# Kernel optimization log

Hardware: AMD Instinct MI355X
Metric: run time of the kernel (lower is better)

Reference implementation:

```python
import jax, jax.numpy as jnp
import numpy as np

# NTM hyperparams (must match init_kwargs)
U = 256        # controller units
N = 128        # memory locations
M = 64         # memory vector size
R = 1          # read heads
WH = 1         # write heads
SHIFT = 1      # conv shift range
S = 2 * SHIFT + 1
OUT = 8        # num_bits_per_vector
CLIP = 20.0
IN_DIM = OUT + 1  # copy task input channels
H = R + WH
PER = M + 1 + 1 + S + 1           # k, beta, g, s, gamma per head
P = H * PER + WH * 2 * M          # + erase/add per write head


def setup_inputs() -> dict:
    key = jax.random.key(0)
    ks = jax.random.split(key, 10)
    B, T = 128, 130
    ctrl_in = IN_DIM + R * M
    def gn(k, shape, fan_in):
        return jax.random.normal(k, shape, jnp.float32) / jnp.sqrt(jnp.float32(fan_in))
    return {
        "inputs": (jax.random.uniform(ks[0], (B, T, IN_DIM)) > 0.5).astype(jnp.float32),
        "W_x": gn(ks[1], (ctrl_in, 4 * U), ctrl_in),
        "W_h": gn(ks[2], (U, 4 * U), U),
        "b_lstm": jnp.zeros((4 * U,), jnp.float32),
        "W_p": gn(ks[3], (U, P), U),
        "b_p": jnp.zeros((P,), jnp.float32),
        "W_o": gn(ks[4], (U + R * M, OUT), U + R * M),
        "b_o": jnp.zeros((OUT,), jnp.float32),
        "r0": jax.random.normal(ks[5], (R, M), jnp.float32) * 0.1,
        "w0": jax.random.normal(ks[6], (H, N), jnp.float32) * 0.1,
        "max_seq_len": 64,
    }


def _ntm_forward(inputs, W_x, W_h, b_lstm, W_p, b_p, W_o, b_o, r0, w0):
    B, T, _ = inputs.shape
    # constant-init memory, learned init read vectors / weightings
    Mem0 = jnp.full((B, N, M), 1e-6, jnp.float32)
    r_prev0 = jnp.broadcast_to(jnp.tanh(r0)[None], (B, R, M))
    w_prev0 = jnp.broadcast_to(jax.nn.softmax(w0, axis=-1)[None], (B, H, N))
    h0 = jnp.zeros((B, U), jnp.float32)
    c0 = jnp.zeros((B, U), jnp.float32)

    def step(carry, x_t):
        h, c, r_prev, w_prev, Mem = carry
        # controller LSTM (input = x_t ++ prev read vectors)
        ctrl_in = jnp.concatenate([x_t, r_prev.reshape(B, R * M)], axis=-1)
        gates = ctrl_in @ W_x + h @ W_h + b_lstm
        i, f, g_, o = jnp.split(gates, 4, axis=-1)
        c = jax.nn.sigmoid(f) * c + jax.nn.sigmoid(i) * jnp.tanh(g_)
        h = jax.nn.sigmoid(o) * jnp.tanh(c)
        # head parameters
        params = jnp.clip(h @ W_p + b_p, -CLIP, CLIP)
        hp = params[:, : H * PER].reshape(B, H, PER)
        k = jnp.tanh(hp[..., :M])                              # [B,H,M]
        beta = jax.nn.softplus(hp[..., M])[..., None]          # [B,H,1]
        g = jax.nn.sigmoid(hp[..., M + 1])[..., None]          # [B,H,1]
        s = jax.nn.softmax(hp[..., M + 2 : M + 2 + S], axis=-1)  # [B,H,S]
        gamma = (1.0 + jax.nn.softplus(hp[..., M + 2 + S]))[..., None]  # [B,H,1]
        ea = params[:, H * PER :].reshape(B, WH, 2, M)
        erase = jax.nn.sigmoid(ea[:, :, 0])                    # [B,WH,M]
        add = jnp.tanh(ea[:, :, 1])                            # [B,WH,M]
        # content addressing: cosine similarity
        inner = jnp.einsum("bhm,bnm->bhn", k, Mem)
        kn = jnp.linalg.norm(k, axis=-1, keepdims=True)        # [B,H,1]
        Mn = jnp.linalg.norm(Mem, axis=-1)[:, None, :]         # [B,1,N]
        K = inner / (kn * Mn + 1e-8)
        w_c = jax.nn.softmax(beta * K, axis=-1)                # [B,H,N]
        # interpolation
        w_g = g * w_c + (1.0 - g) * w_prev
        # circular convolutional shift
        w_tilde = jnp.zeros_like(w_g)
        for d in range(-SHIFT, SHIFT + 1):
            w_tilde = w_tilde + s[..., d + SHIFT : d + SHIFT + 1] * jnp.roll(w_g, d, axis=-1)
        # sharpening
        w_pow = w_tilde ** gamma
        w = w_pow / (jnp.sum(w_pow, axis=-1, keepdims=True) + 1e-8)
        w_r, w_w = w[:, :R], w[:, R:]
        # write (sequential over write heads)
        for j in range(WH):
            ww = w_w[:, j, :, None]                            # [B,N,1]
            Mem = Mem * (1.0 - ww * erase[:, j, None, :]) + ww * add[:, j, None, :]
        # read
        r = jnp.einsum("brn,bnm->brm", w_r, Mem)
        out = jnp.clip(jnp.concatenate([h, r.reshape(B, R * M)], axis=-1) @ W_o + b_o, -CLIP, CLIP)
        return (h, c, r, w, Mem), out

    xs = jnp.swapaxes(inputs, 0, 1)  # [T,B,IN]
    _, outs = jax.lax.scan(step, (h0, c0, r_prev0, w_prev0, Mem0), xs)
    return jnp.swapaxes(outs, 0, 1)  # [B,T,OUT]


def reference(inputs, W_x, W_h, b_lstm, W_p, b_p, W_o, b_o, r0, w0, max_seq_len):
    seq = _ntm_forward(inputs, W_x, W_h, b_lstm, W_p, b_p, W_o, b_o, r0, w0)
    logits = seq[:, max_seq_len + 1 :, :]  # copy task slice
    return jax.nn.sigmoid(logits)
```

## Files before the change

kernel.cpp:

```cpp
#include <hip/hip_runtime.h>
#include <math.h>

typedef _Float16 h2_t __attribute__((ext_vector_type(2)));

#define U_ 256
#define NN 128
#define MM 64
#define OUT_ 8
#define CLIPV 20.0f
#define IN_DIM_ 9
#define PP 268
#define B_ 128
#define T_ 130
#define TSTART 65

#define NWX2 10240
#define NWH8 16384
#define NWP8 4352
#define WX2_OFF 0
#define WH8_OFF 163840
#define WP8_OFF 425984
#define BLH_OFF 495616
#define BPP_OFF 499712
#define COMM_OFF 500800
#define COMM_STRIDE 2176
#define COMM_SZ (B_*COMM_STRIDE)
#define PREP_N (NWX2 + NWH8 + NWP8 + 256 + 272)

#define WSCALE 256.f
#define HSCALE 127.f
#define OSCALE (1.f/(256.f*127.f))

__device__ __forceinline__ float sigf(float x){ return 1.0f/(1.0f+__expf(-x)); }
__device__ __forceinline__ float splus(float x){ return log1pf(__expf(x)); }
__device__ __forceinline__ float clipf(float x){ return fminf(fmaxf(x,-CLIPV),CLIPV); }

#if defined(__has_builtin)
#if __has_builtin(__builtin_amdgcn_fdot2)
#define DOT2(a,b,c) __builtin_amdgcn_fdot2((a),(b),(c),false)
#endif
#endif
#ifndef DOT2
#define DOT2(a,b,c) fmaf((float)(a).x,(float)(b).x, fmaf((float)(a).y,(float)(b).y,(c)))
#endif

#if defined(__has_builtin)
#if __has_builtin(__builtin_amdgcn_sdot4)
#define SDOT4(a,b,c) __builtin_amdgcn_sdot4((a),(b),(c),false)
#endif
#endif
#ifndef SDOT4
__device__ __forceinline__ int sdot4_sw(int a, int b, int c){
    c += (int)(signed char)(a      ) * (int)(signed char)(b      );
    c += (int)(signed char)(a >> 8 ) * (int)(signed char)(b >> 8 );
    c += (int)(signed char)(a >> 16) * (int)(signed char)(b >> 16);
    c += (a >> 24) * (b >> 24);
    return c;
}
#define SDOT4(a,b,c) sdot4_sw((a),(b),(c))
#endif

#define DOT2X4(uu, hv) { \
    a0 = DOT2(hv, __builtin_bit_cast(h2_t,(uu).x), a0); \
    a1 = DOT2(hv, __builtin_bit_cast(h2_t,(uu).y), a1); \
    a2 = DOT2(hv, __builtin_bit_cast(h2_t,(uu).z), a2); \
    a3 = DOT2(hv, __builtin_bit_cast(h2_t,(uu).w), a3); }
#define SD4(u, hw) { \
    a0 = SDOT4((int)(u).x, hw, a0); a1 = SDOT4((int)(u).y, hw, a1); \
    a2 = SDOT4((int)(u).z, hw, a2); a3 = SDOT4((int)(u).w, hw, a3); }
#define SD4P(u, hw) { \
    pa0 = SDOT4((int)(u).x, hw, pa0); pa1 = SDOT4((int)(u).y, hw, pa1); \
    pa2 = SDOT4((int)(u).z, hw, pa2); pa3 = SDOT4((int)(u).w, hw, pa3); }
#define H2C(hu) __builtin_bit_cast(h2_t,(hu))

__device__ __forceinline__ unsigned packh2(float a, float b){
    h2_t v; v.x = (_Float16)a; v.y = (_Float16)b;
    return __builtin_bit_cast(unsigned, v);
}

__device__ __forceinline__ unsigned ei8(float w){
    int v = (int)rintf(w * WSCALE);
    v = v < -127 ? -127 : (v > 127 ? 127 : v);
    return (unsigned)(v & 0xFF);
}

__device__ __forceinline__ unsigned packi8x4(float a, float b, float c, float d){
    int va = (int)rintf(a * HSCALE); va = va < -127 ? -127 : (va > 127 ? 127 : va);
    int vb = (int)rintf(b * HSCALE); vb = vb < -127 ? -127 : (vb > 127 ? 127 : vb);
    int vc = (int)rintf(c * HSCALE); vc = vc < -127 ? -127 : (vc > 127 ? 127 : vc);
    int vd = (int)rintf(d * HSCALE); vd = vd < -127 ? -127 : (vd > 127 ? 127 : vd);
    return (va & 0xFF) | ((vb & 0xFF) << 8) | ((vc & 0xFF) << 16) | ((vd & 0xFF) << 24);
}

__global__ void prep_kernel(const float* __restrict__ W_x, const float* __restrict__ W_h,
                            const float* __restrict__ W_p, const float* __restrict__ b_lstm,
                            const float* __restrict__ b_p,
                            uint4* __restrict__ wx2, uint4* __restrict__ whi8,
                            uint4* __restrict__ wpi8,
                            float4* __restrict__ blh, float* __restrict__ bpp)
{
    for (int idx = blockIdx.x*blockDim.x + threadIdx.x; idx < PREP_N; idx += gridDim.x*blockDim.x){
        if (idx < NWX2){
            int hf = idx/5120, rem = idx - hf*5120;
            int wv = rem/320, r2 = rem - wv*320, p = r2>>6, ln = r2&63;
            int g4 = wv*8 + (ln>>3), q = ln&7, kk = q*5+p;
            int k0 = 2*kk, k1 = k0+1;
            unsigned c[4];
            #pragma unroll
            for (int g=0; g<4; ++g){
                int col = g*256 + hf*128 + g4;
                float f0 = (k0<64) ? W_x[(9+k0)*1024+col] : (k0<73 ? W_x[(k0-64)*1024+col] : 0.f);
                float f1 = (k1<64) ? W_x[(9+k1)*1024+col] : (k1<73 ? W_x[(k1-64)*1024+col] : 0.f);
                c[g] = packh2(f0,f1);
            }
            wx2[idx] = make_uint4(c[0],c[1],c[2],c[3]);
        } else if (idx < NWX2 + NWH8){
            int e = idx - NWX2;
            int hf = e>>13, rem = e&8191, g4 = rem>>6, s = rem&63;
            int j = s>>3, q = s&7, kb = q*32 + 4*j;
            unsigned c[4];
            #pragma unroll
            for (int g=0; g<4; ++g){
                int col = g*256 + hf*128 + g4;
                c[g] = ei8(W_h[(kb+0)*1024+col])
                     | (ei8(W_h[(kb+1)*1024+col]) << 8)
                     | (ei8(W_h[(kb+2)*1024+col]) << 16)
                     | (ei8(W_h[(kb+3)*1024+col]) << 24);
            }
            whi8[e] = make_uint4(c[0],c[1],c[2],c[3]);
        } else if (idx < NWX2 + NWH8 + NWP8){
            int e = idx - NWX2 - NWH8;
            int cg = e>>6, s = e&63;
            int j = s>>3, q = s&7, kb = q*32 + 4*j;
            unsigned c[4];
            #pragma unroll
            for (int g=0; g<4; ++g){
                int cl = cg*4+g;
                if (cl < PP){
                    c[g] = ei8(W_p[(kb+0)*PP+cl])
                         | (ei8(W_p[(kb+1)*PP+cl]) << 8)
                         | (ei8(W_p[(kb+2)*PP+cl]) << 16)
                         | (ei8(W_p[(kb+3)*PP+cl]) << 24);
                } else c[g] = 0u;
            }
            wpi8[e] = make_uint4(c[0],c[1],c[2],c[3]);
        } else if (idx < NWX2 + NWH8 + NWP8 + 256){
            int u = idx - NWX2 - NWH8 - NWP8;
            blh[u] = make_float4(b_lstm[u], b_lstm[256+u], b_lstm[512+u], b_lstm[768+u]);
        } else {
            int j = idx - NWX2 - NWH8 - NWP8 - 256;
            bpp[j] = (j < PP) ? b_p[j] : 0.f;
        }
    }
}

__device__ __forceinline__ float decodeP(int rc, float p){
    if (rc < 64 || (rc >= 70 && rc < 134) || rc >= 204) return tanhf(p);
    if (rc >= 140 && rc < 204) return sigf(p);
    return p;
}

__global__ __launch_bounds__(1024,1) void ntm_kernel(
    const float* __restrict__ inputs,
    const float* __restrict__ W_o, const float* __restrict__ b_o,
    const float* __restrict__ r0, const float* __restrict__ w0,
    const uint4* __restrict__ wx2, const uint4* __restrict__ whi8,
    const uint4* __restrict__ wpi8,
    const float4* __restrict__ blh, const float* __restrict__ bpp,
    char* comm, float* __restrict__ out)
{
    const int bid = blockIdx.x, hf = bid>>7, b = bid&127;
    const int t = threadIdx.x, wv = t>>6, ln = t&63;
    const int g4 = t>>3, q = t&7;

    char* cb = comm + b*COMM_STRIDE;
    volatile float* hOwn = (volatile float*)(cb + hf*512);
    volatile float* hOth = (volatile float*)(cb + (hf^1)*512);
    volatile int*   flg  = (volatile int*)(cb + 2112);

    __shared__ uint4 wxL[5120];
    __shared__ uint4 whL8[2][1024];
    __shared__ float Mem[NN][MM+1];
    __shared__ float4 gpart4[128];
    __shared__ float4 blhL[128];
    __shared__ float hbuf[U_];
    __shared__ float cbuf[128];
    __shared__ unsigned hq[64];
    __shared__ h2_t  xr2[40] __attribute__((aligned(16)));
    __shared__ float prmS[12];
    __shared__ float scal[12];
    __shared__ float kv[2][MM], ebuf[MM], abuf[MM];
    __shared__ float innr[2][NN], Mn[NN], wgs[2][NN], wtab[2][NN];
    __shared__ float rpart[16][MM];
    __shared__ float jpart[OUT_];

    for (int i=t; i<5120; i+=1024) wxL[i] = wx2[hf*5120 + i];
    for (int i=t; i<2048; i+=1024){
        int j = i>>10, jj = i&1023;
        whL8[j][jj] = whi8[hf*8192 + (jj>>3)*64 + j*8 + (jj&7)];
    }
    for (int i=t; i<NN*MM; i+=1024) Mem[i>>6][i&63] = 1e-6f;
    if (t < 128){
        gpart4[t] = make_float4(0.f,0.f,0.f,0.f);
        blhL[t] = blh[hf*128+t];
        cbuf[t] = 0.f;
        Mn[t] = 8e-6f;
    }
    if (t < 64) hq[t] = 0u;
    if (t < U_) hbuf[t] = 0.f;
    if (t >= 128 && t < 256){
        int h = (t-128)>>6, l = t&63;
        float v0 = w0[h*NN + l], v1 = w0[h*NN + l + 64];
        float mx = fmaxf(v0,v1);
        for (int off=32; off>=1; off>>=1) mx = fmaxf(mx, __shfl_xor(mx, off));
        float e0 = __expf(v0-mx), e1 = __expf(v1-mx);
        float s = e0+e1;
        for (int off=32; off>=1; off>>=1) s += __shfl_xor(s, off);
        wtab[h][l] = e0/s; wtab[h][l+64] = e1/s;
    }
    if (t >= 256 && t < 296){
        int p = t-256;
        h2_t v;
        if (p < 32){ v.x = (_Float16)tanhf(r0[2*p]); v.y = (_Float16)tanhf(r0[2*p+1]); }
        else if (p < 37){
            int e0 = 2*(p-32), e1 = e0+1;
            float f0 = (e0<IN_DIM_) ? inputs[b*T_*IN_DIM_ + e0] : 0.f;
            float f1 = (e1<IN_DIM_) ? inputs[b*T_*IN_DIM_ + e1] : 0.f;
            v.x = (_Float16)f0; v.y = (_Float16)f1;
        } else { v.x=(_Float16)0.f; v.y=(_Float16)0.f; }
        xr2[p] = v;
    }
    __syncthreads();

    for (int step=0; step<T_; ++step){
        {
            const uint4* wb = wxL + wv*320;
            float a0=0.f,a1=0.f,a2=0.f,a3=0.f;
            #pragma unroll
            for (int p=0; p<5; ++p){
                uint4 u = wb[p*64 + ln];
                h2_t xv = xr2[q*5+p];
                DOT2X4(u, xv);
            }
            #pragma unroll
            for (int m=1; m<8; m<<=1){
                a0 += __shfl_xor(a0,m); a1 += __shfl_xor(a1,m);
                a2 += __shfl_xor(a2,m); a3 += __shfl_xor(a3,m);
            }
            if (q==0){
                float4 bb = blhL[g4]; float4 gp = gpart4[g4];
                float gi=a0+bb.x+gp.x, gf=a1+bb.y+gp.y, gg=a2+bb.z+gp.z, go=a3+bb.w+gp.w;
                float c = sigf(gf)*cbuf[g4] + sigf(gi)*tanhf(gg);
                cbuf[g4] = c;
                float h = sigf(go)*tanhf(c);
                hbuf[hf*128+g4] = h;
                hOwn[g4] = h;
            }
        }
        __syncthreads();
        if (t==0){
            flg[hf] = step+1;
            while (flg[hf^1] < step+1) __builtin_amdgcn_s_sleep(8);
        }
        __syncthreads();
        if (t < 128){
            hbuf[(hf^1)*128 + t] = hOth[t];
        } else if (t < 160){
            const int jj = t-128;
            const float* hp = &hbuf[hf*128 + 4*jj];
            hq[hf*32 + jj] = packi8x4(hp[0], hp[1], hp[2], hp[3]);
        } else if (t < 192){
            const int jj = t-160;
            float h0 = hOth[4*jj], h1 = hOth[4*jj+1], h2 = hOth[4*jj+2], h3 = hOth[4*jj+3];
            hq[(hf^1)*32 + jj] = packi8x4(h0, h1, h2, h3);
        }
        __syncthreads();

        const int* hqi = (const int*)hq;

        {
            const uint4* wrow = whi8 + hf*8192 + g4*64;
            int a0=0,a1=0,a2=0,a3=0;
            uint4 s2 = wrow[16+q], s3 = wrow[24+q], s4 = wrow[32+q];
            uint4 s5 = wrow[40+q], s6 = wrow[48+q], s7 = wrow[56+q];
            uint4 l0 = whL8[0][t], l1 = whL8[1][t];
            int hw0=hqi[q*8+0], hw1=hqi[q*8+1], hw2=hqi[q*8+2], hw3=hqi[q*8+3];
            int hw4=hqi[q*8+4], hw5=hqi[q*8+5], hw6=hqi[q*8+6], hw7=hqi[q*8+7];
            SD4(l0, hw0); SD4(l1, hw1);
            SD4(s2, hw2); SD4(s3, hw3);
            SD4(s4, hw4); SD4(s5, hw5);
            SD4(s6, hw6); SD4(s7, hw7);
            #pragma unroll
            for (int m=1; m<8; m<<=1){
                a0 += __shfl_xor(a0,m); a1 += __shfl_xor(a1,m);
                a2 += __shfl_xor(a2,m); a3 += __shfl_xor(a3,m);
            }
            if (q==0) gpart4[g4] = make_float4(a0*OSCALE, a1*OSCALE, a2*OSCALE, a3*OSCALE);
        }
        if (t < 544){
            const int cg = t>>3, qq = t&7;
            const uint4* wrow = wpi8 + cg*64;
            int pa0=0, pa1=0, pa2=0, pa3=0;
            uint4 u0=wrow[0*8+qq], u1=wrow[1*8+qq], u2=wrow[2*8+qq], u3=wrow[3*8+qq];
            uint4 u4=wrow[4*8+qq], u5=wrow[5*8+qq], u6=wrow[6*8+qq], u7=wrow[7*8+qq];
            int hw0=hqi[qq*8+0], hw1=hqi[qq*8+1], hw2=hqi[qq*8+2], hw3=hqi[qq*8+3];
            int hw4=hqi[qq*8+4], hw5=hqi[qq*8+5], hw6=hqi[qq*8+6], hw7=hqi[qq*8+7];
            SD4P(u0, hw0); SD4P(u1, hw1);
            SD4P(u2, hw2); SD4P(u3, hw3);
            SD4P(u4, hw4); SD4P(u5, hw5);
            SD4P(u6, hw6); SD4P(u7, hw7);
            #pragma unroll
            for (int m=1; m<8; m<<=1){
                pa0 += __shfl_xor(pa0,m); pa1 += __shfl_xor(pa1,m);
                pa2 += __shfl_xor(pa2,m); pa3 += __shfl_xor(pa3,m);
            }
            if (qq==0){
                #pragma unroll
                for (int j=0; j<4; ++j){
                    int aj = (j==0)?pa0:((j==1)?pa1:((j==2)?pa2:pa3));
                    int cl = cg*4+j;
                    if (cl < PP){
                        float pv = clipf(aj*OSCALE + bpp[cl]);
                        float dv = decodeP(cl, pv);
                        if (cl < 64) kv[0][cl] = dv;
                        else if (cl < 70) prmS[cl-64] = dv;
                        else if (cl < 134) kv[1][cl-70] = dv;
                        else if (cl < 140) prmS[6+cl-134] = dv;
                        else if (cl < 204) ebuf[cl-140] = dv;
                        else abuf[cl-204] = dv;
                    }
                }
            }
        } else if (t < 800){
            const int idx = t-544, n = idx>>1, m0 = (idx&1)*32;
            float s = 0.f;
            #pragma unroll 8
            for (int m=m0; m<m0+32; ++m){ float v=Mem[n][m]; s=fmaf(v,v,s); }
            s += __shfl_xor(s,1);
            if (!(idx&1)) Mn[n] = sqrtf(s);
        } else if (t < 928){
            const int o = (t-800)>>4, l16 = (t-800)&15;
            float s = 0.f;
            #pragma unroll
            for (int j=0; j<16; ++j){
                const int i = l16 + (j<<4);
                s = fmaf(hbuf[i], W_o[i*OUT_ + o], s);
            }
            s += __shfl_xor(s,1); s += __shfl_xor(s,2);
            s += __shfl_xor(s,4); s += __shfl_xor(s,8);
            if (l16==0) jpart[o] = s;
        } else if (t < 933){
            if (step+1 < T_){
                const int p = t-928;
                const int e0 = 2*p, e1 = e0+1;
                const float* xin = inputs + (b*T_ + step+1)*IN_DIM_;
                h2_t v;
                v.x = (_Float16)((e0<IN_DIM_) ? xin[e0] : 0.f);
                v.y = (_Float16)((e1<IN_DIM_) ? xin[e1] : 0.f);
                xr2[32+p] = v;
            }
        }
        __syncthreads();

        {
            const int h = t>>9, n = (t>>2)&127, qm = t&3, m0 = qm*16;
            float s = 0.f;
            #pragma unroll 8
            for (int m=m0; m<m0+16; ++m) s = fmaf(kv[h][m], Mem[n][m], s);
            s += __shfl_xor(s,1); s += __shfl_xor(s,2);
            if (qm==0) innr[h][n] = s;
        }
        if (t < 2){
            const int h = t;
            const float* ps = prmS + 6*h;
            scal[h]   = splus(ps[0]);
            scal[2+h] = sigf(ps[1]);
            float p0=ps[2], p1=ps[3], p2=ps[4];
            float mx = fmaxf(p0, fmaxf(p1, p2));
            float e0=__expf(p0-mx), e1=__expf(p1-mx), e2=__expf(p2-mx);
            float s = e0+e1+e2;
            scal[6+3*h]=e0/s; scal[7+3*h]=e1/s; scal[8+3*h]=e2/s;
            scal[4+h] = 1.f + splus(ps[5]);
        }
        __syncthreads();

        if (t < 128){
            const int h = t>>6, l = ln;
            float kvl = kv[h][l];
            float kn2 = kvl*kvl;
            for (int off=32; off>=1; off>>=1) kn2 += __shfl_xor(kn2, off);
            float kn = sqrtf(kn2);
            float beta = scal[h], g = scal[2+h];
            float bk0 = beta * innr[h][l]   /(kn*Mn[l]   +1e-8f);
            float bk1 = beta * innr[h][l+64]/(kn*Mn[l+64]+1e-8f);
            float mx = fmaxf(bk0,bk1);
            for (int off=32; off>=1; off>>=1) mx = fmaxf(mx, __shfl_xor(mx, off));
            float e0=__expf(bk0-mx), e1=__expf(bk1-mx);
            float s=e0+e1;
            for (int off=32; off>=1; off>>=1) s += __shfl_xor(s, off);
            float wc0=e0/s, wc1=e1/s;
            wgs[h][l]    = g*wc0 + (1.f-g)*wtab[h][l];
            wgs[h][l+64] = g*wc1 + (1.f-g)*wtab[h][l+64];
            float gamma = scal[4+h];
            float s0=scal[6+3*h], s1=scal[7+3*h], s2=scal[8+3*h];
            const int n0=l, n1=l+64;
            float wt0 = s0*wgs[h][(n0+1)&127] + s1*wgs[h][n0] + s2*wgs[h][(n0+127)&127];
            float wt1 = s0*wgs[h][(n1+1)&127] + s1*wgs[h][n1] + s2*wgs[h][(n1+127)&127];
            float wp0 = __powf(wt0, gamma), wp1 = __powf(wt1, gamma);
            float ss = wp0+wp1;
            for (int off=32; off>=1; off>>=1) ss += __shfl_xor(ss, off);
            float inv = 1.0f/(ss+1e-8f);
            wtab[h][n0] = wp0*inv; wtab[h][n1] = wp1*inv;
        }
        __syncthreads();

        {
            const float el = ebuf[ln], al = abuf[ln];
            const int n0 = wv*8;
            float racc = 0.f;
            #pragma unroll
            for (int k=0; k<8; ++k){
                const int n = n0+k;
                float ww = wtab[1][n];
                float wr = wtab[0][n];
                float v = Mem[n][ln]*(1.0f - ww*el) + ww*al;
                Mem[n][ln] = v;
                racc = fmaf(wr, v, racc);
            }
            rpart[wv][ln] = racc;
        }
        __syncthreads();

        if (t < 512){
            const int o = wv;
            float rm = 0.f;
            #pragma unroll
            for (int k=0; k<16; ++k) rm += rpart[k][ln];
            float s = rm * W_o[(U_+ln)*OUT_ + o];
            for (int off=32; off>=1; off>>=1) s += __shfl_xor(s, off);
            if (ln==0 && hf==0 && step>=TSTART){
                float logit = clipf(s + jpart[o] + b_o[o]);
                out[((b*(T_-TSTART)) + (step-TSTART))*OUT_ + o] = sigf(logit);
            }
        } else if (t < 576){
            float rm = 0.f;
            #pragma unroll
            for (int k=0; k<16; ++k) rm += rpart[k][ln];
            float other = __shfl_xor(rm, 1);
            if (!(ln&1)){
                h2_t v; v.x = (_Float16)rm; v.y = (_Float16)other;
                xr2[ln>>1] = v;
            }
        }
        __syncthreads();
    }
}

extern "C" void kernel_launch(void* const* d_in, const int* in_sizes, int n_in,
                              void* d_out, int out_size, void* d_ws, size_t ws_size,
                              hipStream_t stream) {
    const float* inputs = (const float*)d_in[0];
    const float* W_x    = (const float*)d_in[1];
    const float* W_h    = (const float*)d_in[2];
    const float* b_lstm = (const float*)d_in[3];
    const float* W_p    = (const float*)d_in[4];
    const float* b_p    = (const float*)d_in[5];
    const float* W_o    = (const float*)d_in[6];
    const float* b_o    = (const float*)d_in[7];
    const float* r0     = (const float*)d_in[8];
    const float* w0     = (const float*)d_in[9];
    float* out = (float*)d_out;

    char* ws = (char*)d_ws;
    uint4*  wx2 = (uint4*)(ws + WX2_OFF);
    uint4*  wh8 = (uint4*)(ws + WH8_OFF);
    uint4*  wp8 = (uint4*)(ws + WP8_OFF);
    float4* blh = (float4*)(ws + BLH_OFF);
    float*  bpp = (float*)(ws + BPP_OFF);
    char*   comm = ws + COMM_OFF;

    hipMemsetAsync(comm, 0, COMM_SZ, stream);
    prep_kernel<<<512, 256, 0, stream>>>(W_x, W_h, W_p, b_lstm, b_p, wx2, wh8, wp8, blh, bpp);
    ntm_kernel<<<2*B_, 1024, 0, stream>>>(inputs, W_o, b_o, r0, w0,
                                          wx2, wh8, wp8, blh, bpp, comm, out);
}
```

Before: 1.613 ms.

## Quantize input/read-vector LSTM weights to int8 and stage more W_h in LDS

Changes the x/read-vector part of the LSTM gate matmul from fp16 dot2 to int8 sdot4. Weights are quantized in the prep kernel, and the read vector and input are packed as int8 with the same scales as the recurrent path. This cuts LDS footprint and per-step dot instructions. The freed LDS is used to stage half of W_h in shared memory (four slices instead of two), reducing global/L2 loads per step. It also shortens the cross-block spin sleep, at the cost of extra quantization error on the read vector and input path.

```diff
diff --git a/kernel.cpp b/kernel.cpp
--- a/kernel.cpp
+++ b/kernel.cpp
@@ -14,18 +14,18 @@
 #define T_ 130
 #define TSTART 65
 
-#define NWX2 10240
+#define NWXI 6144
 #define NWH8 16384
 #define NWP8 4352
-#define WX2_OFF 0
-#define WH8_OFF 163840
-#define WP8_OFF 425984
-#define BLH_OFF 495616
-#define BPP_OFF 499712
-#define COMM_OFF 500800
+#define WXI_OFF 0
+#define WH8_OFF 98304
+#define WP8_OFF 360448
+#define BLH_OFF 430080
+#define BPP_OFF 434176
+#define COMM_OFF 435264
 #define COMM_STRIDE 2176
 #define COMM_SZ (B_*COMM_STRIDE)
-#define PREP_N (NWX2 + NWH8 + NWP8 + 256 + 272)
+#define PREP_N (NWXI + NWH8 + NWP8 + 256 + 272)
 
 #define WSCALE 256.f
 #define HSCALE 127.f
@@ -34,15 +34,6 @@
 __device__ __forceinline__ float sigf(float x){ return 1.0f/(1.0f+__expf(-x)); }
 __device__ __forceinline__ float splus(float x){ return log1pf(__expf(x)); }
 __device__ __forceinline__ float clipf(float x){ return fminf(fmaxf(x,-CLIPV),CLIPV); }
-
-#if defined(__has_builtin)
-#if __has_builtin(__builtin_amdgcn_fdot2)
-#define DOT2(a,b,c) __builtin_amdgcn_fdot2((a),(b),(c),false)
-#endif
-#endif
-#ifndef DOT2
-#define DOT2(a,b,c) fmaf((float)(a).x,(float)(b).x, fmaf((float)(a).y,(float)(b).y,(c)))
-#endif
 
 #if defined(__has_builtin)
 #if __has_builtin(__builtin_amdgcn_sdot4)
@@ -60,23 +51,12 @@
 #define SDOT4(a,b,c) sdot4_sw((a),(b),(c))
 #endif
 
-#define DOT2X4(uu, hv) { \
-    a0 = DOT2(hv, __builtin_bit_cast(h2_t,(uu).x), a0); \
-    a1 = DOT2(hv, __builtin_bit_cast(h2_t,(uu).y), a1); \
-    a2 = DOT2(hv, __builtin_bit_cast(h2_t,(uu).z), a2); \
-    a3 = DOT2(hv, __builtin_bit_cast(h2_t,(uu).w), a3); }
 #define SD4(u, hw) { \
     a0 = SDOT4((int)(u).x, hw, a0); a1 = SDOT4((int)(u).y, hw, a1); \
     a2 = SDOT4((int)(u).z, hw, a2); a3 = SDOT4((int)(u).w, hw, a3); }
 #define SD4P(u, hw) { \
     pa0 = SDOT4((int)(u).x, hw, pa0); pa1 = SDOT4((int)(u).y, hw, pa1); \
     pa2 = SDOT4((int)(u).z, hw, pa2); pa3 = SDOT4((int)(u).w, hw, pa3); }
-#define H2C(hu) __builtin_bit_cast(h2_t,(hu))
-
-__device__ __forceinline__ unsigned packh2(float a, float b){
-    h2_t v; v.x = (_Float16)a; v.y = (_Float16)b;
-    return __builtin_bit_cast(unsigned, v);
-}
 
 __device__ __forceinline__ unsigned ei8(float w){
     int v = (int)rintf(w * WSCALE);
@@ -95,27 +75,31 @@
 __global__ void prep_kernel(const float* __restrict__ W_x, const float* __restrict__ W_h,
                             const float* __restrict__ W_p, const float* __restrict__ b_lstm,
                             const float* __restrict__ b_p,
-                            uint4* __restrict__ wx2, uint4* __restrict__ whi8,
+                            uint4* __restrict__ wxi8, uint4* __restrict__ whi8,
                             uint4* __restrict__ wpi8,
                             float4* __restrict__ blh, float* __restrict__ bpp)
 {
     for (int idx = blockIdx.x*blockDim.x + threadIdx.x; idx < PREP_N; idx += gridDim.x*blockDim.x){
-        if (idx < NWX2){
-            int hf = idx/5120, rem = idx - hf*5120;
-            int wv = rem/320, r2 = rem - wv*320, p = r2>>6, ln = r2&63;
-            int g4 = wv*8 + (ln>>3), q = ln&7, kk = q*5+p;
-            int k0 = 2*kk, k1 = k0+1;
+        if (idx < NWXI){
+            int hf = idx/3072, rem = idx - hf*3072;
+            int wv = rem/192, r2 = rem - wv*192, j = r2>>6, ln = r2&63;
+            int g4 = wv*8 + (ln>>3), q = ln&7, kb = q*12 + 4*j;
             unsigned c[4];
             #pragma unroll
             for (int g=0; g<4; ++g){
                 int col = g*256 + hf*128 + g4;
-                float f0 = (k0<64) ? W_x[(9+k0)*1024+col] : (k0<73 ? W_x[(k0-64)*1024+col] : 0.f);
-                float f1 = (k1<64) ? W_x[(9+k1)*1024+col] : (k1<73 ? W_x[(k1-64)*1024+col] : 0.f);
-                c[g] = packh2(f0,f1);
-            }
-            wx2[idx] = make_uint4(c[0],c[1],c[2],c[3]);
-        } else if (idx < NWX2 + NWH8){
-            int e = idx - NWX2;
+                unsigned w = 0;
+                #pragma unroll
+                for (int k=0; k<4; ++k){
+                    int K = kb+k;
+                    float f = (K<64) ? W_x[(9+K)*1024+col] : (K<73 ? W_x[(K-64)*1024+col] : 0.f);
+                    w |= ei8(f) << (8*k);
+                }
+                c[g] = w;
+            }
+            wxi8[idx] = make_uint4(c[0],c[1],c[2],c[3]);
+        } else if (idx < NWXI + NWH8){
+            int e = idx - NWXI;
             int hf = e>>13, rem = e&8191, g4 = rem>>6, s = rem&63;
             int j = s>>3, q = s&7, kb = q*32 + 4*j;
             unsigned c[4];
@@ -128,8 +112,8 @@
                      | (ei8(W_h[(kb+3)*1024+col]) << 24);
             }
             whi8[e] = make_uint4(c[0],c[1],c[2],c[3]);
-        } else if (idx < NWX2 + NWH8 + NWP8){
-            int e = idx - NWX2 - NWH8;
+        } else if (idx < NWXI + NWH8 + NWP8){
+            int e = idx - NWXI - NWH8;
             int cg = e>>6, s = e&63;
             int j = s>>3, q = s&7, kb = q*32 + 4*j;
             unsigned c[4];
@@ -144,11 +128,11 @@
                 } else c[g] = 0u;
             }
             wpi8[e] = make_uint4(c[0],c[1],c[2],c[3]);
-        } else if (idx < NWX2 + NWH8 + NWP8 + 256){
-            int u = idx - NWX2 - NWH8 - NWP8;
+        } else if (idx < NWXI + NWH8 + NWP8 + 256){
+            int u = idx - NWXI - NWH8 - NWP8;
             blh[u] = make_float4(b_lstm[u], b_lstm[256+u], b_lstm[512+u], b_lstm[768+u]);
         } else {
-            int j = idx - NWX2 - NWH8 - NWP8 - 256;
+            int j = idx - NWXI - NWH8 - NWP8 - 256;
             bpp[j] = (j < PP) ? b_p[j] : 0.f;
         }
     }
@@ -164,7 +148,7 @@
     const float* __restrict__ inputs,
     const float* __restrict__ W_o, const float* __restrict__ b_o,
     const float* __restrict__ r0, const float* __restrict__ w0,
-    const uint4* __restrict__ wx2, const uint4* __restrict__ whi8,
+    const uint4* __restrict__ wxi8, const uint4* __restrict__ whi8,
     const uint4* __restrict__ wpi8,
     const float4* __restrict__ blh, const float* __restrict__ bpp,
     char* comm, float* __restrict__ out)
@@ -178,15 +162,15 @@
     volatile float* hOth = (volatile float*)(cb + (hf^1)*512);
     volatile int*   flg  = (volatile int*)(cb + 2112);
 
-    __shared__ uint4 wxL[5120];
-    __shared__ uint4 whL8[2][1024];
+    __shared__ uint4 wxL8[3072];
+    __shared__ uint4 whL8[4][1024];
     __shared__ float Mem[NN][MM+1];
     __shared__ float4 gpart4[128];
     __shared__ float4 blhL[128];
     __shared__ float hbuf[U_];
     __shared__ float cbuf[128];
     __shared__ unsigned hq[64];
-    __shared__ h2_t  xr2[40] __attribute__((aligned(16)));
+    __shared__ unsigned xq[24];
     __shared__ float prmS[12];
     __shared__ float scal[12];
     __shared__ float kv[2][MM], ebuf[MM], abuf[MM];
@@ -194,8 +178,8 @@
     __shared__ float rpart[16][MM];
     __shared__ float jpart[OUT_];
 
-    for (int i=t; i<5120; i+=1024) wxL[i] = wx2[hf*5120 + i];
-    for (int i=t; i<2048; i+=1024){
+    for (int i=t; i<3072; i+=1024) wxL8[i] = wxi8[hf*3072 + i];
+    for (int i=t; i<4096; i+=1024){
         int j = i>>10, jj = i&1023;
         whL8[j][jj] = whi8[hf*8192 + (jj>>3)*64 + j*8 + (jj&7)];
     }
@@ -218,29 +202,33 @@
         for (int off=32; off>=1; off>>=1) s += __shfl_xor(s, off);
         wtab[h][l] = e0/s; wtab[h][l+64] = e1/s;
     }
-    if (t >= 256 && t < 296){
+    if (t >= 256 && t < 280){
         int p = t-256;
-        h2_t v;
-        if (p < 32){ v.x = (_Float16)tanhf(r0[2*p]); v.y = (_Float16)tanhf(r0[2*p+1]); }
-        else if (p < 37){
-            int e0 = 2*(p-32), e1 = e0+1;
-            float f0 = (e0<IN_DIM_) ? inputs[b*T_*IN_DIM_ + e0] : 0.f;
-            float f1 = (e1<IN_DIM_) ? inputs[b*T_*IN_DIM_ + e1] : 0.f;
-            v.x = (_Float16)f0; v.y = (_Float16)f1;
-        } else { v.x=(_Float16)0.f; v.y=(_Float16)0.f; }
-        xr2[p] = v;
+        if (p < 16){
+            xq[p] = packi8x4(tanhf(r0[4*p]), tanhf(r0[4*p+1]), tanhf(r0[4*p+2]), tanhf(r0[4*p+3]));
+        } else if (p < 19){
+            const float* xin = inputs + b*T_*IN_DIM_;
+            int e0 = 4*(p-16);
+            float f0 = (e0+0<IN_DIM_) ? xin[e0+0] : 0.f;
+            float f1 = (e0+1<IN_DIM_) ? xin[e0+1] : 0.f;
+            float f2 = (e0+2<IN_DIM_) ? xin[e0+2] : 0.f;
+            float f3 = (e0+3<IN_DIM_) ? xin[e0+3] : 0.f;
+            xq[p] = packi8x4(f0,f1,f2,f3);
+        } else xq[p] = 0u;
     }
     __syncthreads();
 
     for (int step=0; step<T_; ++step){
+        const int* xqi = (const int*)xq;
+
         {
-            const uint4* wb = wxL + wv*320;
-            float a0=0.f,a1=0.f,a2=0.f,a3=0.f;
-            #pragma unroll
-            for (int p=0; p<5; ++p){
-                uint4 u = wb[p*64 + ln];
-                h2_t xv = xr2[q*5+p];
-                DOT2X4(u, xv);
+            const uint4* wb = wxL8 + wv*192;
+            int a0=0,a1=0,a2=0,a3=0;
+            #pragma unroll
+            for (int j=0; j<3; ++j){
+                uint4 u = wb[j*64 + ln];
+                int xw = xqi[q*3+j];
+                SD4(u, xw);
             }
             #pragma unroll
             for (int m=1; m<8; m<<=1){
@@ -249,7 +237,8 @@
             }
             if (q==0){
                 float4 bb = blhL[g4]; float4 gp = gpart4[g4];
-                float gi=a0+bb.x+gp.x, gf=a1+bb.y+gp.y, gg=a2+bb.z+gp.z, go=a3+bb.w+gp.w;
+                float gi=a0*OSCALE+bb.x+gp.x, gf=a1*OSCALE+bb.y+gp.y;
+                float gg=a2*OSCALE+bb.z+gp.z, go=a3*OSCALE+bb.w+gp.w;
                 float c = sigf(gf)*cbuf[g4] + sigf(gi)*tanhf(gg);
                 cbuf[g4] = c;
                 float h = sigf(go)*tanhf(c);
@@ -260,7 +249,7 @@
         __syncthreads();
         if (t==0){
             flg[hf] = step+1;
-            while (flg[hf^1] < step+1) __builtin_amdgcn_s_sleep(8);
+            while (flg[hf^1] < step+1) __builtin_amdgcn_s_sleep(2);
         }
         __syncthreads();
         if (t < 128){
@@ -281,13 +270,12 @@
         {
             const uint4* wrow = whi8 + hf*8192 + g4*64;
             int a0=0,a1=0,a2=0,a3=0;
-            uint4 s2 = wrow[16+q], s3 = wrow[24+q], s4 = wrow[32+q];
-            uint4 s5 = wrow[40+q], s6 = wrow[48+q], s7 = wrow[56+q];
-            uint4 l0 = whL8[0][t], l1 = whL8[1][t];
+            uint4 s4 = wrow[32+q], s5 = wrow[40+q], s6 = wrow[48+q], s7 = wrow[56+q];
+            uint4 l0 = whL8[0][t], l1 = whL8[1][t], l2 = whL8[2][t], l3 = whL8[3][t];
             int hw0=hqi[q*8+0], hw1=hqi[q*8+1], hw2=hqi[q*8+2], hw3=hqi[q*8+3];
             int hw4=hqi[q*8+4], hw5=hqi[q*8+5], hw6=hqi[q*8+6], hw7=hqi[q*8+7];
             SD4(l0, hw0); SD4(l1, hw1);
-            SD4(s2, hw2); SD4(s3, hw3);
+            SD4(l2, hw2); SD4(l3, hw3);
             SD4(s4, hw4); SD4(s5, hw5);
             SD4(s6, hw6); SD4(s7, hw7);
             #pragma unroll
@@ -349,15 +337,16 @@
             s += __shfl_xor(s,1); s += __shfl_xor(s,2);
             s += __shfl_xor(s,4); s += __shfl_xor(s,8);
             if (l16==0) jpart[o] = s;
-        } else if (t < 933){
+        } else if (t < 931){
             if (step+1 < T_){
                 const int p = t-928;
-                const int e0 = 2*p, e1 = e0+1;
                 const float* xin = inputs + (b*T_ + step+1)*IN_DIM_;
-                h2_t v;
-                v.x = (_Float16)((e0<IN_DIM_) ? xin[e0] : 0.f);
-                v.y = (_Float16)((e1<IN_DIM_) ? xin[e1] : 0.f);
-                xr2[32+p] = v;
+                int e0 = 4*p;
+                float f0 = (e0+0<IN_DIM_) ? xin[e0+0] : 0.f;
+                float f1 = (e0+1<IN_DIM_) ? xin[e0+1] : 0.f;
+                float f2 = (e0+2<IN_DIM_) ? xin[e0+2] : 0.f;
+                float f3 = (e0+3<IN_DIM_) ? xin[e0+3] : 0.f;
+                xq[16+p] = packi8x4(f0,f1,f2,f3);
             }
         }
         __syncthreads();
@@ -446,11 +435,10 @@
             float rm = 0.f;
             #pragma unroll
             for (int k=0; k<16; ++k) rm += rpart[k][ln];
-            float other = __shfl_xor(rm, 1);
-            if (!(ln&1)){
-                h2_t v; v.x = (_Float16)rm; v.y = (_Float16)other;
-                xr2[ln>>1] = v;
-            }
+            float r1 = __shfl_down(rm, 1);
+            float r2 = __shfl_down(rm, 2);
+            float r3 = __shfl_down(rm, 3);
+            if (!(ln&3)) xq[ln>>2] = packi8x4(rm, r1, r2, r3);
         }
         __syncthreads();
     }
@@ -472,7 +460,7 @@
     float* out = (float*)d_out;
 
     char* ws = (char*)d_ws;
-    uint4*  wx2 = (uint4*)(ws + WX2_OFF);
+    uint4*  wxi = (uint4*)(ws + WXI_OFF);
     uint4*  wh8 = (uint4*)(ws + WH8_OFF);
     uint4*  wp8 = (uint4*)(ws + WP8_OFF);
     float4* blh = (float4*)(ws + BLH_OFF);
@@ -480,7 +468,7 @@
     char*   comm = ws + COMM_OFF;
 
     hipMemsetAsync(comm, 0, COMM_SZ, stream);
-    prep_kernel<<<512, 256, 0, stream>>>(W_x, W_h, W_p, b_lstm, b_p, wx2, wh8, wp8, blh, bpp);
+    prep_kernel<<<512, 256, 0, stream>>>(W_x, W_h, W_p, b_lstm, b_p, wxi, wh8, wp8, blh, bpp);
     ntm_kernel<<<2*B_, 1024, 0, stream>>>(inputs, W_o, b_o, r0, w0,
-                                          wx2, wh8, wp8, blh, bpp, comm, out);
-}
+                                          wxi, wh8, wp8, blh, bpp, comm, out);
+}
```

After: 1.559 ms, median of 2. -3.4%, faster.
